# Optimization experiments

Measured on AMD Instinct MI355X. Metric: run time of the kernel, lower is better.

Reference implementation:

```python
import jax, jax.numpy as jnp
import numpy as np

N = 50000      # nodes
E = 800000     # edges (avg degree 16)
D = 64         # num_hidden
H = 4          # heads
OUT = 64       # out_dim

def setup_inputs() -> dict:
    key = jax.random.key(0)
    k = jax.random.split(key, 5)
    h = jax.random.normal(k[0], (N, D), dtype=jnp.float32)
    edge_index = jax.random.randint(k[1], (2, E), 0, N)
    gate_w = jax.random.normal(k[2], (H, 2 * D), dtype=jnp.float32) * 0.1  # per-head gate Linear weight
    gate_b = jnp.zeros((H,), dtype=jnp.float32)
    W_cat = jax.random.normal(k[3], (OUT, H * D), dtype=jnp.float32) * 0.05
    b_cat = jnp.zeros((OUT,), dtype=jnp.float32)
    return dict(h=h, edge_index=edge_index, gate_w=gate_w, gate_b=gate_b, W_cat=W_cat, b_cat=b_cat)

def reference(h, edge_index, gate_w, gate_b, W_cat, b_cat):
    # eval mode: both dropouts are identity
    row, col = edge_index[0], edge_index[1]
    n, d = h.shape
    # symmetric-ish degree normalization based on out-degree of row (as in original)
    deg = jax.ops.segment_sum(jnp.ones((row.shape[0],), dtype=h.dtype), row, num_segments=n)
    nd = jnp.clip(deg, 1.0) ** -0.5                     # [N]
    hr = h[row]                                          # [E, D] gather (source)
    hc = h[col]                                          # [E, D] gather (target)
    # per-head gate: tanh(Linear(cat(hr, hc))) vectorized over heads
    w1 = gate_w[:, :d]                                   # [H, D]
    w2 = gate_w[:, d:]                                   # [H, D]
    g = jnp.tanh(hr @ w1.T + hc @ w2.T + gate_b)        # [E, H]
    norm = g * (nd[row] * nd[col])[:, None]              # [E, H]
    # message: norm * x_j where x_j = h[source] = hr; aggregate (add) at target = col
    msgs = norm[:, :, None] * hr[:, None, :]             # [E, H, D]
    agg = jax.ops.segment_sum(msgs, col, num_segments=n) # [N, H, D]
    res = agg.reshape(n, -1)                             # concat heads -> [N, H*D]
    return jax.nn.relu(res @ W_cat.T + b_cat)            # [N, OUT]
```

## Files before the change

kernel.cpp:

```cpp
#include <hip/hip_runtime.h>

#define DD 64
#define HH 4
#define OUTC 64
#define CAP 48
#define CHUNK 2048
#define KB 5

typedef __attribute__((ext_vector_type(8))) short bf16x8;
typedef __attribute__((ext_vector_type(4))) float f32x4;

__device__ __forceinline__ float fast_tanh(float x) {
    x = fminf(fmaxf(x, -15.f), 15.f);
    float e = __expf(2.f * x);
    return 1.f - 2.f / (e + 1.f);
}

__device__ __forceinline__ unsigned short f2bf(float f) {
    unsigned int u = __float_as_uint(f);
    u = (u + 0x7FFFu + ((u >> 16) & 1u)) >> 16;
    return (unsigned short)u;
}

__global__ __launch_bounds__(256) void partition_kernel(const int* __restrict__ row,
                                                        const int* __restrict__ col,
                                                        unsigned* __restrict__ cbuck,
                                                        unsigned char* __restrict__ rbuck,
                                                        int* __restrict__ ccount,
                                                        int* __restrict__ rcount,
                                                        int E, int NBUK, int BCAP, int nchunks) {
    __shared__ int hist[256];
    __shared__ int scn[256];
    __shared__ int gbase[256];
    __shared__ unsigned stage[CHUNK];
    __shared__ int saddr[CHUNK];
    int tid = threadIdx.x;
    int phaseC = (blockIdx.x < nchunks) ? 1 : 0;
    int chunk = phaseC ? blockIdx.x : blockIdx.x - nchunks;
    int e0 = chunk * CHUNK;
    int n = E - e0;
    if (n > CHUNK) n = CHUNK;
    const int* key = phaseC ? col : row;

    hist[tid] = 0;
    __syncthreads();
    for (int i = tid; i < n; i += 256) atomicAdd(&hist[key[e0 + i] >> 8], 1);
    __syncthreads();
    int v = hist[tid];
    scn[tid] = v;
    __syncthreads();
    for (int d = 1; d < 256; d <<= 1) {
        int a = (tid >= d) ? scn[tid - d] : 0;
        __syncthreads();
        scn[tid] += a;
        __syncthreads();
    }
    int excl = scn[tid] - v;
    scn[tid] = excl;
    if (tid < NBUK && v > 0)
        gbase[tid] = tid * BCAP + atomicAdd(phaseC ? &ccount[tid] : &rcount[tid], v);
    else
        gbase[tid] = tid * BCAP;
    hist[tid] = 0;
    __syncthreads();

    if (phaseC) {
        for (int i = tid; i < n; i += 256) {
            int c = col[e0 + i];
            int r = row[e0 + i];
            int b = c >> 8;
            int k = atomicAdd(&hist[b], 1);
            int p = scn[b] + k;
            stage[p] = ((unsigned)r << 8) | (unsigned)(c & 255);
            saddr[p] = gbase[b] + k;
        }
        __syncthreads();
        for (int i = tid; i < n; i += 256) cbuck[saddr[i]] = stage[i];
    } else {
        unsigned char* stB = (unsigned char*)stage;
        for (int i = tid; i < n; i += 256) {
            int r = row[e0 + i];
            int b = r >> 8;
            int k = atomicAdd(&hist[b], 1);
            int p = scn[b] + k;
            stB[p] = (unsigned char)(r & 255);
            saddr[p] = gbase[b] + k;
        }
        __syncthreads();
        for (int i = tid; i < n; i += 256) rbuck[saddr[i]] = stB[i];
    }
}

#define HSTR 68
__global__ __launch_bounds__(256) void local_prep(const unsigned* __restrict__ cbuck,
                                                  const unsigned char* __restrict__ rbuck,
                                                  const int* __restrict__ ccount,
                                                  const int* __restrict__ rcount,
                                                  int* __restrict__ cnt,
                                                  unsigned short* __restrict__ slots,
                                                  float* __restrict__ nd,
                                                  const float* __restrict__ h,
                                                  const float* __restrict__ gate_w,
                                                  const float* __restrict__ gate_b,
                                                  const float* __restrict__ Wcat,
                                                  float* __restrict__ a12,
                                                  unsigned short* __restrict__ hbs,
                                                  unsigned short* __restrict__ WTbf,
                                                  int N, int NBUK, int BCAP) {
    __shared__ char smem[38400];
    int tid = threadIdx.x;
    int b = blockIdx.x;
    if (b == 3 * NBUK) {
        for (int i = tid; i < 2048; i += 256) {
            int ln = i & 63;
            int ks = (i >> 6) & 7;
            int ct = i >> 9;
            int o = ct * 16 + (ln & 15);
            int kb = ks * 32 + ((ln >> 4) & 3) * 8;
            const float4* src = (const float4*)&Wcat[(size_t)o * 256 + kb];
            float4 w0 = src[0];
            float4 w1 = src[1];
            ushort4* dst = (ushort4*)&WTbf[(size_t)i * 8];
            dst[0] = make_ushort4(f2bf(w0.x), f2bf(w0.y), f2bf(w0.z), f2bf(w0.w));
            dst[1] = make_ushort4(f2bf(w1.x), f2bf(w1.y), f2bf(w1.z), f2bf(w1.w));
        }
        return;
    }
    int* cur = (int*)smem;
    cur[tid] = 0;
    __syncthreads();
    if (b < NBUK) {
        unsigned short* slds = (unsigned short*)(smem + 1024);
        int s = ccount[b];
        if (s > BCAP) s = BCAP;
        const unsigned* src = cbuck + (size_t)b * BCAP;
        int node0 = b << 8;
        for (int i = tid; i < s; i += 256) {
            unsigned rc = src[i];
            int cl = rc & 255;
            int k = atomicAdd(&cur[cl], 1);
            if (k < CAP) slds[cl * CAP + k] = (unsigned short)(rc >> 8);
        }
        __syncthreads();
        int node = node0 + tid;
        if (node < N) cnt[node] = cur[tid];
        uint4* gdst = (uint4*)(slots + (size_t)node0 * CAP);
        const uint4* gsrc = (const uint4*)slds;
        for (int i = tid; i < 1536; i += 256) gdst[i] = gsrc[i];
    } else {
        float* gws = (float*)(smem + 1024);
        float* ndf = (float*)(smem + 3072);
        float* hs = (float*)(smem + 3584);
        int idx = b - NBUK;
        int bb = idx >> 1;
        int half = idx & 1;
        int node0h = (bb << 8) + half * 128;
        int s = rcount[bb];
        if (s > BCAP) s = BCAP;
        const unsigned char* src = rbuck + (size_t)bb * BCAP;
        for (int i = tid; i < s; i += 256) atomicAdd(&cur[src[i]], 1);
        for (int i = tid; i < 512; i += 256) gws[i] = gate_w[i];
        int nn = N - node0h;
        if (nn > 128) nn = 128;
        if (nn < 0) nn = 0;
        int tile4 = nn * 16;
        const float4* hsrc = (const float4*)(h + (size_t)node0h * DD);
        for (int i = tid; i < tile4; i += 256) {
            int j = i >> 4, q = i & 15;
            *(float4*)&hs[j * HSTR + q * 4] = hsrc[i];
        }
        __syncthreads();
        if (tid < nn) {
            int dg = cur[half * 128 + tid];
            float ndv = rsqrtf((float)(dg < 1 ? 1 : dg));
            nd[node0h + tid] = ndv;
            ndf[tid] = ndv;
        }
        __syncthreads();
        int j = tid >> 1, sel = tid & 1;
        if (j < nn) {
            float acc[4];
            acc[0] = acc[1] = acc[2] = acc[3] = 0.f;
            const float4* hrow = (const float4*)&hs[j * HSTR];
#pragma unroll
            for (int q = 0; q < 16; ++q) {
                float4 hv = hrow[q];
#pragma unroll
                for (int m = 0; m < 4; ++m) {
                    float4 gv = *(const float4*)&gws[(sel * 4 + m) * 64 + q * 4];
                    acc[m] += hv.x * gv.x + hv.y * gv.y + hv.z * gv.z + hv.w * gv.w;
                }
            }
            int node = node0h + j;
#pragma unroll
            for (int m = 0; m < 4; ++m) {
                int mm = sel * 4 + m;
                int hd = mm >> 1, part = mm & 1;
                float vv = acc[m] + (part == 0 ? gate_b[hd] : 0.f);
                a12[(size_t)node * 8 + part * 4 + hd] = vv;
            }
        }
        for (int i = tid; i < tile4; i += 256) {
            int j2 = i >> 4, q = i & 15;
            float sc = ndf[j2];
            const float* p = &hs[j2 * HSTR + q * 4];
            ushort4 pv;
            pv.x = f2bf(sc * p[0]);
            pv.y = f2bf(sc * p[1]);
            pv.z = f2bf(sc * p[2]);
            pv.w = f2bf(sc * p[3]);
            *(ushort4*)&hbs[(size_t)(node0h + j2) * DD + q * 4] = pv;
        }
    }
}

__global__ __launch_bounds__(256) void gg_kernel(const int* __restrict__ cnt,
                                                 const unsigned short* __restrict__ slots,
                                                 const float* __restrict__ nd,
                                                 const float* __restrict__ a12,
                                                 const unsigned short* __restrict__ hbs,
                                                 const unsigned short* __restrict__ WTbf,
                                                 const float* __restrict__ b_cat,
                                                 float* __restrict__ out, int N) {
    __shared__ char glds[4 * (KB * 1024 + 640)];
    __shared__ unsigned short A2[16 * 264];
    int tid = threadIdx.x;
    int wv = tid >> 6;
    int lane = tid & 63;
    int quad = lane >> 4;
    int mcol = lane & 15;
    float bb = b_cat[wv * 16 + mcol];

    char* Alds = glds + wv * (KB * 1024 + 640);
    unsigned short* Au = (unsigned short*)Alds;
    int* rlds = (int*)(Alds + KB * 1024);

    int n0 = blockIdx.x << 4;
    int c0 = n0 + wv * 4;
    int o1, o2, o3, o4;
    {
        int l0 = (c0 + 0 < N) ? cnt[c0 + 0] : 0; if (l0 > CAP) l0 = CAP;
        int l1 = (c0 + 1 < N) ? cnt[c0 + 1] : 0; if (l1 > CAP) l1 = CAP;
        int l2 = (c0 + 2 < N) ? cnt[c0 + 2] : 0; if (l2 > CAP) l2 = CAP;
        int l3 = (c0 + 3 < N) ? cnt[c0 + 3] : 0; if (l3 > CAP) l3 = CAP;
        o1 = l0; o2 = o1 + l1; o3 = o2 + l2; o4 = o3 + l3;
    }
    int K = o4;
    int tksteps = (K + 31) >> 5;
    f32x4 acc0 = (f32x4){0.f, 0.f, 0.f, 0.f};
    f32x4 acc1 = (f32x4){0.f, 0.f, 0.f, 0.f};
    f32x4 acc2 = (f32x4){0.f, 0.f, 0.f, 0.f};
    f32x4 acc3 = (f32x4){0.f, 0.f, 0.f, 0.f};

    for (int kb0 = 0; kb0 < tksteps; kb0 += KB) {
        int bks = tksteps - kb0;
        if (bks > KB) bks = KB;
        int kstart = kb0 << 5;
        int kend = kstart + (bks << 5);
        if (kend > K) kend = K;
        for (int z = lane; z < bks * 256; z += 64) ((unsigned*)Au)[z] = 0u;
        for (int z = lane; z < bks * 32; z += 64) rlds[z] = 0;
        for (int p = kstart + lane; p < kend; p += 64) {
            int i = (p >= o1) + (p >= o2) + (p >= o3);
            int c = c0 + i;
            int off = p - (i == 0 ? 0 : (i == 1 ? o1 : (i == 2 ? o2 : o3)));
            int r = slots[(size_t)c * CAP + off];
            int pl = p - kstart;
            rlds[pl] = r;
            float4 a1 = *(const float4*)&a12[(size_t)r * 8];
            float4 a2 = *(const float4*)&a12[(size_t)c * 8 + 4];
            float t0 = fast_tanh(a1.x + a2.x);
            float t1 = fast_tanh(a1.y + a2.y);
            float t2 = fast_tanh(a1.z + a2.z);
            float t3 = fast_tanh(a1.w + a2.w);
            int bidx = (pl >> 5) * 512 + ((pl >> 3) & 3) * 128 + (pl & 7);
            int m0 = i * 4;
            Au[bidx + (m0 + 0) * 8] = f2bf(t0);
            Au[bidx + (m0 + 1) * 8] = f2bf(t1);
            Au[bidx + (m0 + 2) * 8] = f2bf(t2);
            Au[bidx + (m0 + 3) * 8] = f2bf(t3);
        }
        for (int ks = 0; ks < bks; ++ks) {
            bf16x8 af = *(const bf16x8*)(Alds + ks * 1024 + lane * 16);
            int rk[8];
#pragma unroll
            for (int j = 0; j < 8; ++j) rk[j] = rlds[ks * 32 + quad * 8 + j];
#pragma unroll
            for (int nt = 0; nt < 4; ++nt) {
                const unsigned short* hp = hbs + nt * 16 + mcol;
                bf16x8 bf;
#pragma unroll
                for (int j = 0; j < 8; ++j) bf[j] = (short)hp[(size_t)rk[j] << 6];
                if (nt == 0) acc0 = __builtin_amdgcn_mfma_f32_16x16x32_bf16(af, bf, acc0, 0, 0, 0);
                else if (nt == 1) acc1 = __builtin_amdgcn_mfma_f32_16x16x32_bf16(af, bf, acc1, 0, 0, 0);
                else if (nt == 2) acc2 = __builtin_amdgcn_mfma_f32_16x16x32_bf16(af, bf, acc2, 0, 0, 0);
                else acc3 = __builtin_amdgcn_mfma_f32_16x16x32_bf16(af, bf, acc3, 0, 0, 0);
            }
        }
    }
    {
        int node = c0 + quad;
        int nl = wv * 4 + quad;
        float ndv = (node < N) ? nd[node] : 0.f;
        unsigned short* dst = &A2[nl * 264 + mcol];
#pragma unroll
        for (int reg = 0; reg < 4; ++reg) {
            dst[reg * 64 + 0] = f2bf(acc0[reg] * ndv);
            dst[reg * 64 + 16] = f2bf(acc1[reg] * ndv);
            dst[reg * 64 + 32] = f2bf(acc2[reg] * ndv);
            dst[reg * 64 + 48] = f2bf(acc3[reg] * ndv);
        }
    }
    __syncthreads();
    {
        f32x4 c4 = (f32x4){0.f, 0.f, 0.f, 0.f};
#pragma unroll
        for (int ks = 0; ks < 8; ++ks) {
            bf16x8 af = *(const bf16x8*)&A2[mcol * 264 + ks * 32 + quad * 8];
            bf16x8 bf = *(const bf16x8*)&WTbf[(size_t)((wv * 8 + ks) * 64 + lane) * 8];
            c4 = __builtin_amdgcn_mfma_f32_16x16x32_bf16(af, bf, c4, 0, 0, 0);
        }
#pragma unroll
        for (int reg = 0; reg < 4; ++reg) {
            int n = n0 + quad * 4 + reg;
            if (n < N) {
                float v = c4[reg] + bb;
                out[(size_t)n * OUTC + wv * 16 + mcol] = v > 0.f ? v : 0.f;
            }
        }
    }
}

extern "C" void kernel_launch(void* const* d_in, const int* in_sizes, int n_in,
                              void* d_out, int out_size, void* d_ws, size_t ws_size,
                              hipStream_t stream) {
    const float* h      = (const float*)d_in[0];
    const int*   edge   = (const int*)d_in[1];
    const float* gate_w = (const float*)d_in[2];
    const float* gate_b = (const float*)d_in[3];
    const float* Wcat   = (const float*)d_in[4];
    const float* b_cat  = (const float*)d_in[5];
    int N = in_sizes[0] / DD;
    int E = in_sizes[1] / 2;
    const int* row = edge;
    const int* colp = edge + E;
    float* out = (float*)d_out;

    int NBUK = (N + 255) >> 8;
    int BCAP = ((2 * E / NBUK) + 63) & ~63;

    char* ws = (char*)d_ws;
    size_t off = 0;
    size_t pad = ((size_t)NBUK * 4 + 255) & ~255ull;
    int*   ccount = (int*)(ws + off); off += pad;
    int*   rcount = (int*)(ws + off); off += pad;
    int*   cnt    = (int*)(ws + off); off += (size_t)N * 4;
    float* nd     = (float*)(ws + off); off += (size_t)N * 4;
    float* a12    = (float*)(ws + off); off += (size_t)N * 32;
    unsigned short* slots = (unsigned short*)(ws + off);
    off += ((size_t)NBUK * 256 * CAP * 2 + 255) & ~255ull;
    unsigned short* hbs  = (unsigned short*)(ws + off); off += (size_t)N * DD * 2;
    unsigned short* WTbf = (unsigned short*)(ws + off); off += 2048 * 8 * 2;
    char* scratch = ws + off;
    unsigned*      cbuck = (unsigned*)scratch;
    unsigned char* rbuck = (unsigned char*)(scratch + (size_t)NBUK * BCAP * 4);

    hipMemsetAsync(ccount, 0, pad + (size_t)NBUK * 4, stream);

    int nchunks = (E + CHUNK - 1) / CHUNK;
    partition_kernel<<<2 * nchunks, 256, 0, stream>>>(row, colp, cbuck, rbuck, ccount, rcount,
                                                      E, NBUK, BCAP, nchunks);
    local_prep<<<3 * NBUK + 1, 256, 0, stream>>>(cbuck, rbuck, ccount, rcount, cnt, slots, nd,
                                                 h, gate_w, gate_b, Wcat, a12, hbs, WTbf,
                                                 N, NBUK, BCAP);
    int ntiles = (N + 15) >> 4;
    gg_kernel<<<ntiles, 256, 0, stream>>>(cnt, slots, nd, a12, hbs, WTbf, b_cat, out, N);
}
```

Measured before the change: 132.1 us.

## Interleave bf16 feature layout so each lane gathers four columns in one 8-byte load

The scaled bf16 copy of h is now stored with columns interleaved (q, 16+q, 32+q, 48+q) so that the four MFMA column tiles a lane needs sit next to each other. The gather in gg_kernel then issues one 8-byte load per source row instead of four separate 2-byte loads, cutting the number of scattered global memory transactions by four. The cost is some extra bit unpacking in registers, and the producer and consumer layouts must stay in sync.

```diff
diff --git a/kernel.cpp b/kernel.cpp
--- a/kernel.cpp
+++ b/kernel.cpp
@@ -203,12 +203,12 @@
         for (int i = tid; i < tile4; i += 256) {
             int j2 = i >> 4, q = i & 15;
             float sc = ndf[j2];
-            const float* p = &hs[j2 * HSTR + q * 4];
+            const float* p = &hs[j2 * HSTR];
             ushort4 pv;
-            pv.x = f2bf(sc * p[0]);
-            pv.y = f2bf(sc * p[1]);
-            pv.z = f2bf(sc * p[2]);
-            pv.w = f2bf(sc * p[3]);
+            pv.x = f2bf(sc * p[q]);
+            pv.y = f2bf(sc * p[16 + q]);
+            pv.z = f2bf(sc * p[32 + q]);
+            pv.w = f2bf(sc * p[48 + q]);
             *(ushort4*)&hbs[(size_t)(node0h + j2) * DD + q * 4] = pv;
         }
     }
@@ -285,17 +285,22 @@
             int rk[8];
 #pragma unroll
             for (int j = 0; j < 8; ++j) rk[j] = rlds[ks * 32 + quad * 8 + j];
-#pragma unroll
-            for (int nt = 0; nt < 4; ++nt) {
-                const unsigned short* hp = hbs + nt * 16 + mcol;
-                bf16x8 bf;
-#pragma unroll
-                for (int j = 0; j < 8; ++j) bf[j] = (short)hp[(size_t)rk[j] << 6];
-                if (nt == 0) acc0 = __builtin_amdgcn_mfma_f32_16x16x32_bf16(af, bf, acc0, 0, 0, 0);
-                else if (nt == 1) acc1 = __builtin_amdgcn_mfma_f32_16x16x32_bf16(af, bf, acc1, 0, 0, 0);
-                else if (nt == 2) acc2 = __builtin_amdgcn_mfma_f32_16x16x32_bf16(af, bf, acc2, 0, 0, 0);
-                else acc3 = __builtin_amdgcn_mfma_f32_16x16x32_bf16(af, bf, acc3, 0, 0, 0);
+            uint2 bv[8];
+#pragma unroll
+            for (int j = 0; j < 8; ++j)
+                bv[j] = *(const uint2*)&hbs[((size_t)rk[j] << 6) + mcol * 4];
+            bf16x8 b0, b1, b2, b3;
+#pragma unroll
+            for (int j = 0; j < 8; ++j) {
+                b0[j] = (short)(bv[j].x & 0xFFFFu);
+                b1[j] = (short)(bv[j].x >> 16);
+                b2[j] = (short)(bv[j].y & 0xFFFFu);
+                b3[j] = (short)(bv[j].y >> 16);
             }
+            acc0 = __builtin_amdgcn_mfma_f32_16x16x32_bf16(af, b0, acc0, 0, 0, 0);
+            acc1 = __builtin_amdgcn_mfma_f32_16x16x32_bf16(af, b1, acc1, 0, 0, 0);
+            acc2 = __builtin_amdgcn_mfma_f32_16x16x32_bf16(af, b2, acc2, 0, 0, 0);
+            acc3 = __builtin_amdgcn_mfma_f32_16x16x32_bf16(af, b3, acc3, 0, 0, 0);
         }
     }
     {
```

Measured after the change: 132.3 us. About the same (+0.1%).
